# Optimization experiments

Hardware: AMD Instinct MI355X
Metric: run time of the kernel (lower is better)

## Reference

```python
import jax, jax.numpy as jnp
import numpy as np

NUM_NODES = 1024; NGRAPH = 16; N = NUM_NODES * NGRAPH
DEG = 16; E_RAND = N * DEG
F_IN = 16; EMB = 64; H = 4; C = 64; DM = H * C  # 256
NHEAD = 2; DH = DM // NHEAD; FF = 1024; OUT = 1024; NEXTRA = 3


def _p(key, shape, scale=0.05):
    return scale * jax.random.normal(key, shape, jnp.float32)


def setup_inputs() -> dict:
    key = jax.random.key(0)
    ks = iter(jax.random.split(key, 64))
    x = jax.random.normal(next(ks), (N, F_IN), jnp.float32)
    src = jax.random.randint(next(ks), (E_RAND,), 0, N, jnp.int32)
    dst = jax.random.randint(next(ks), (E_RAND,), 0, N, jnp.int32)
    loop = jnp.arange(N, dtype=jnp.int32)  # PyG GATConv add_self_loops=True
    d = {
        'x': x,
        'edge_src': jnp.concatenate([src, loop]),
        'edge_dst': jnp.concatenate([dst, loop]),
        'batch': (jnp.arange(N) // NUM_NODES).astype(jnp.int32),
        'fc1_W': _p(next(ks), (F_IN, EMB)), 'fc1_b': jnp.zeros((EMB,), jnp.float32),
        'g0_W': _p(next(ks), (EMB, DM)), 'g0_as': _p(next(ks), (H, C)),
        'g0_ad': _p(next(ks), (H, C)), 'g0_b': jnp.zeros((DM,), jnp.float32),
        'gW': _p(next(ks), (NEXTRA, DM, DM)), 'gas': _p(next(ks), (NEXTRA, H, C)),
        'gad': _p(next(ks), (NEXTRA, H, C)), 'gb': jnp.zeros((NEXTRA, DM), jnp.float32),
        'sa_Wq': _p(next(ks), (DM, DM)), 'sa_bq': jnp.zeros((DM,), jnp.float32),
        'sa_Wk': _p(next(ks), (DM, DM)), 'sa_bk': jnp.zeros((DM,), jnp.float32),
        'sa_Wv': _p(next(ks), (DM, DM)), 'sa_bv': jnp.zeros((DM,), jnp.float32),
        'sa_Wo': _p(next(ks), (DM, DM)), 'sa_bo': jnp.zeros((DM,), jnp.float32),
        'ca_Wq': _p(next(ks), (DM, DM)), 'ca_bq': jnp.zeros((DM,), jnp.float32),
        'ca_Wk': _p(next(ks), (DM, DM)), 'ca_bk': jnp.zeros((DM,), jnp.float32),
        'ca_Wv': _p(next(ks), (DM, DM)), 'ca_bv': jnp.zeros((DM,), jnp.float32),
        'ca_Wo': _p(next(ks), (DM, DM)), 'ca_bo': jnp.zeros((DM,), jnp.float32),
        'ln1_g': jnp.ones((DM,), jnp.float32), 'ln1_b': jnp.zeros((DM,), jnp.float32),
        'ln2_g': jnp.ones((DM,), jnp.float32), 'ln2_b': jnp.zeros((DM,), jnp.float32),
        'ln3_g': jnp.ones((DM,), jnp.float32), 'ln3_b': jnp.zeros((DM,), jnp.float32),
        'ff1_W': _p(next(ks), (DM, FF)), 'ff1_b': jnp.zeros((FF,), jnp.float32),
        'ff2_W': _p(next(ks), (FF, DM)), 'ff2_b': jnp.zeros((DM,), jnp.float32),
        'fc_W': _p(next(ks), (DM, OUT)), 'fc_b': jnp.zeros((OUT,), jnp.float32),
    }
    return d


def reference(x, edge_src, edge_dst, batch, fc1_W, fc1_b, g0_W, g0_as, g0_ad, g0_b,
              gW, gas, gad, gb,
              sa_Wq, sa_bq, sa_Wk, sa_bk, sa_Wv, sa_bv, sa_Wo, sa_bo,
              ca_Wq, ca_bq, ca_Wk, ca_bk, ca_Wv, ca_bv, ca_Wo, ca_bo,
              ln1_g, ln1_b, ln2_g, ln2_b, ln3_g, ln3_b,
              ff1_W, ff1_b, ff2_W, ff2_b, fc_W, fc_b):
    n = x.shape[0]

    def gat(h_in, W, a_s, a_d, b):
        h = (h_in @ W).reshape(n, H, C)                                  # [N,H,C]
        e = jax.nn.leaky_relu((h * a_s).sum(-1)[edge_src]
                              + (h * a_d).sum(-1)[edge_dst], 0.2)        # [E,H]
        m = jax.ops.segment_max(e, edge_dst, num_segments=n)
        p = jnp.exp(e - m[edge_dst])
        denom = jax.ops.segment_sum(p, edge_dst, num_segments=n)
        alpha = p / (denom[edge_dst] + 1e-16)
        out = jax.ops.segment_sum(alpha[:, :, None] * h[edge_src], edge_dst,
                                  num_segments=n)                        # [N,H,C]
        return out.reshape(n, DM) + b

    def ln(v, g, b):
        mu = v.mean(-1, keepdims=True)
        var = v.var(-1, keepdims=True)
        return (v - mu) / jnp.sqrt(var + 1e-5) * g + b

    def mha(q_in, kv_in, Wq, bq, Wk, bk, Wv, bv, Wo, bo):
        Bq, S, _ = q_in.shape
        q = (q_in @ Wq + bq).reshape(Bq, S, NHEAD, DH)
        k = (kv_in @ Wk + bk).reshape(Bq, -1, NHEAD, DH)
        v = (kv_in @ Wv + bv).reshape(Bq, -1, NHEAD, DH)
        att = jax.nn.softmax(jnp.einsum('bqhd,bkhd->bhqk', q, k) / np.float32(np.sqrt(DH)), axis=-1)
        o = jnp.einsum('bhqk,bkhd->bqhd', att, v).reshape(Bq, S, DM)
        return o @ Wo + bo

    h = x @ fc1_W + fc1_b
    h = jax.nn.leaky_relu(gat(h, g0_W, g0_as, g0_ad, g0_b), 0.01)
    for i in range(NEXTRA):
        h = jax.nn.leaky_relu(gat(h, gW[i], gas[i], gad[i], gb[i]), 0.01)

    t = h.reshape(NGRAPH, NUM_NODES, DM)
    mem = t
    t = ln(t + mha(t, t, sa_Wq, sa_bq, sa_Wk, sa_bk, sa_Wv, sa_bv, sa_Wo, sa_bo), ln1_g, ln1_b)
    t = ln(t + mha(t, mem, ca_Wq, ca_bq, ca_Wk, ca_bk, ca_Wv, ca_bv, ca_Wo, ca_bo), ln2_g, ln2_b)
    t = ln(t + (jax.nn.relu(t @ ff1_W + ff1_b) @ ff2_W + ff2_b), ln3_g, ln3_b)

    h = t.reshape(n, DM)
    cnt = jax.ops.segment_sum(jnp.ones((n,), h.dtype), batch, num_segments=NGRAPH)
    pooled = jax.ops.segment_sum(h, batch, num_segments=NGRAPH) / cnt[:, None]
    return pooled @ fc_W + fc_b
```

## Files before the change

### kernel.cpp

```cpp
#include <hip/hip_runtime.h>
#include <cstddef>

#define NNODES 16384
#define DMODEL 256
#define CCH 64
#define SQLEN 1024
#define NGRAPH 16
#define ADH 128

typedef __bf16 bf16;
typedef __attribute__((ext_vector_type(8))) __bf16 bf16x8;
typedef __attribute__((ext_vector_type(4))) __bf16 bf16x4;
typedef __attribute__((ext_vector_type(4))) float floatx4;

template <int BN>
__global__ __launch_bounds__(256) void mfma_gemm_t(
    const bf16* __restrict__ A, const bf16* __restrict__ Bt,
    const float* __restrict__ bias, float* __restrict__ Cf, bf16* __restrict__ Cb,
    int M, int N, int K, int act,
    const float* __restrict__ gas, const float* __restrict__ gad,
    float* __restrict__ ssrc, float* __restrict__ sdst)
{
  constexpr int BM = 128;
  constexpr int MW = (BN == 128) ? 4 : 2;
  constexpr int NW = 4;
  constexpr int ACH = BM / 8;
  constexpr int TCH = (BM + BN) / 8;
  __shared__ bf16 As[BM * 64];
  __shared__ bf16 Bs[BN * 64];
  const int tid = threadIdx.x;
  const int wave = tid >> 6, lane = tid & 63;
  const int m0 = blockIdx.y * BM, n0 = blockIdx.x * BN;
  const int lr = lane & 15, quad = lane >> 4;
  const int wm = (BN == 128) ? (wave >> 1) * 64 : wave * 32;
  const int wn = (BN == 128) ? (wave & 1) * 64 : 0;
  const int r8 = lane >> 3, cu = lane & 7;
  const int scol = (cu ^ r8) * 8;

  floatx4 acc[MW][NW];
  const floatx4 zero = {0.f, 0.f, 0.f, 0.f};
#pragma unroll
  for (int i = 0; i < MW; i++)
#pragma unroll
    for (int j = 0; j < NW; j++) acc[i][j] = zero;

  for (int k0 = 0; k0 < K; k0 += 64) {
#pragma unroll
    for (int c = wave; c < TCH; c += 4) {
      const bf16* g;
      bf16* l;
      if (c < ACH) {
        g = A + (size_t)(m0 + c * 8 + r8) * K + k0 + scol;
        l = &As[c * 512];
      } else {
        int c2 = c - ACH;
        g = Bt + (size_t)(n0 + c2 * 8 + r8) * K + k0 + scol;
        l = &Bs[c2 * 512];
      }
      __builtin_amdgcn_global_load_lds(
          (const __attribute__((address_space(1))) void*)g,
          (__attribute__((address_space(3))) void*)l, 16, 0, 0);
    }
    __syncthreads();
#pragma unroll
    for (int ks = 0; ks < 2; ks++) {
      bf16x8 af[MW], bfr[NW];
#pragma unroll
      for (int i = 0; i < MW; i++) {
        int row = wm + i * 16 + lr;
        af[i] = *(const bf16x8*)&As[(row * 8 + ((ks * 4 + quad) ^ (row & 7))) * 8];
      }
#pragma unroll
      for (int i = 0; i < NW; i++) {
        int row = wn + i * 16 + lr;
        bfr[i] = *(const bf16x8*)&Bs[(row * 8 + ((ks * 4 + quad) ^ (row & 7))) * 8];
      }
#pragma unroll
      for (int mi = 0; mi < MW; mi++)
#pragma unroll
        for (int ni = 0; ni < NW; ni++)
          acc[mi][ni] = __builtin_amdgcn_mfma_f32_16x16x32_bf16(af[mi], bfr[ni], acc[mi][ni], 0, 0, 0);
    }
    __syncthreads();
  }

  float as_v[4], ad_v[4];
  int head = 0;
  if (gas) {
    head = (n0 + wn) >> 6;
#pragma unroll
    for (int ni = 0; ni < 4; ni++) {
      as_v[ni] = gas[head * 64 + ni * 16 + lr];
      ad_v[ni] = gad[head * 64 + ni * 16 + lr];
    }
  }

#pragma unroll
  for (int mi = 0; mi < MW; mi++) {
    int rbase = m0 + wm + mi * 16 + quad * 4;
#pragma unroll
    for (int r = 0; r < 4; r++) {
      int row = rbase + r;
      float s1 = 0.f, s2 = 0.f;
#pragma unroll
      for (int ni = 0; ni < NW; ni++) {
        int col = n0 + wn + ni * 16 + lr;
        float v = acc[mi][ni][r];
        if (gas) { s1 += v * as_v[ni]; s2 += v * ad_v[ni]; }
        if (bias) v += bias[col];
        if (act == 1) v = fmaxf(v, 0.f);
        if (Cf) Cf[(size_t)row * N + col] = v;
        if (Cb) Cb[(size_t)row * N + col] = (bf16)v;
      }
      if (gas) {
        s1 += __shfl_xor(s1, 1); s1 += __shfl_xor(s1, 2);
        s1 += __shfl_xor(s1, 4); s1 += __shfl_xor(s1, 8);
        s2 += __shfl_xor(s2, 1); s2 += __shfl_xor(s2, 2);
        s2 += __shfl_xor(s2, 4); s2 += __shfl_xor(s2, 8);
        if (lr == 0) {
          ssrc[row * 4 + head] = s1;
          sdst[row * 4 + head] = s2;
        }
      }
    }
  }
}

struct PrepArgs {
  const float* sq[11]; bf16* dq[11];
  const float* g0W; bf16* g0Wt;
  const float* ff1W; bf16* ff1Wt;
  const float* ff2W; bf16* ff2Wt;
  const float* sabq; const float* sabk; const float* sabv;
  const float* cabk; const float* cabv;
  float* qkvb; float* kvb;
  int* cnt;
  const float* x; const float* fc1W; const float* fc1b; bf16* h0;
};

__global__ __launch_bounds__(256) void prep_kernel(PrepArgs a)
{
  __shared__ float t[32][33];
  int b = blockIdx.x;
  int tid = threadIdx.x;
  int tx = tid & 31, ty = tid >> 5;
  if (b < 704) {
    int w = b >> 6, tile = b & 63;
    int n0 = (tile & 7) * 32, k0 = (tile >> 3) * 32;
    const float* W = a.sq[w];
    bf16* Wt = a.dq[w];
#pragma unroll
    for (int i = 0; i < 4; i++) t[ty + 8 * i][tx] = W[(size_t)(k0 + ty + 8 * i) * 256 + n0 + tx];
    __syncthreads();
#pragma unroll
    for (int i = 0; i < 4; i++) Wt[(size_t)(n0 + ty + 8 * i) * 256 + k0 + tx] = (bf16)t[tx][ty + 8 * i];
  } else if (b < 720) {
    int tile = b - 704;
    int n0 = (tile & 7) * 32, k0 = (tile >> 3) * 32;
#pragma unroll
    for (int i = 0; i < 4; i++) t[ty + 8 * i][tx] = a.g0W[(size_t)(k0 + ty + 8 * i) * 256 + n0 + tx];
    __syncthreads();
#pragma unroll
    for (int i = 0; i < 4; i++) a.g0Wt[(size_t)(n0 + ty + 8 * i) * 64 + k0 + tx] = (bf16)t[tx][ty + 8 * i];
  } else if (b < 976) {
    int tile = b - 720;
    int n0 = (tile & 31) * 32, k0 = (tile >> 5) * 32;
#pragma unroll
    for (int i = 0; i < 4; i++) t[ty + 8 * i][tx] = a.ff1W[(size_t)(k0 + ty + 8 * i) * 1024 + n0 + tx];
    __syncthreads();
#pragma unroll
    for (int i = 0; i < 4; i++) a.ff1Wt[(size_t)(n0 + ty + 8 * i) * 256 + k0 + tx] = (bf16)t[tx][ty + 8 * i];
  } else if (b < 1232) {
    int tile = b - 976;
    int n0 = (tile & 7) * 32, k0 = (tile >> 3) * 32;
#pragma unroll
    for (int i = 0; i < 4; i++) t[ty + 8 * i][tx] = a.ff2W[(size_t)(k0 + ty + 8 * i) * 256 + n0 + tx];
    __syncthreads();
#pragma unroll
    for (int i = 0; i < 4; i++) a.ff2Wt[(size_t)(n0 + ty + 8 * i) * 1024 + k0 + tx] = (bf16)t[tx][ty + 8 * i];
  } else if (b == 1232) {
    a.qkvb[tid] = a.sabq[tid];
    a.qkvb[256 + tid] = a.sabk[tid];
    a.qkvb[512 + tid] = a.sabv[tid];
    a.kvb[tid] = a.cabk[tid];
    a.kvb[256 + tid] = a.cabv[tid];
  } else if (b < 1249) {
    int i0 = (b - 1233) * 1024 + tid;
#pragma unroll
    for (int i = 0; i < 4; i++) a.cnt[i0 + 256 * i] = 0;
  } else {
    int idx = (b - 1249) * 256 + tid;
    int n = idx >> 6, j = idx & 63;
    const float* xr = a.x + (size_t)n * 16;
    float s = a.fc1b[j];
#pragma unroll
    for (int k = 0; k < 16; k++) s += xr[k] * a.fc1W[k * 64 + j];
    a.h0[idx] = (bf16)s;
  }
}

__global__ __launch_bounds__(256) void vtrans2_kernel(const bf16* __restrict__ Vc, const bf16* __restrict__ Vs,
                                                      bf16* __restrict__ VtC, bf16* __restrict__ VtS)
{
  __shared__ bf16 t[32][34];
  int z = blockIdx.z;
  const bf16* V;
  bf16* Vt;
  int ldv, coff, b;
  if (z < NGRAPH) { V = Vc; Vt = VtC; ldv = 512; coff = 256; b = z; }
  else            { V = Vs; Vt = VtS; ldv = 768; coff = 512; b = z - NGRAPH; }
  int head = blockIdx.y >> 2, d0 = (blockIdx.y & 3) * 32;
  int k0 = blockIdx.x * 32;
  int tx = threadIdx.x & 31, ty = threadIdx.x >> 5;
#pragma unroll
  for (int i = 0; i < 4; i++)
    t[ty + 8 * i][tx] = V[((size_t)(b * SQLEN + k0 + ty + 8 * i)) * ldv + coff + head * ADH + d0 + tx];
  __syncthreads();
#pragma unroll
  for (int i = 0; i < 4; i++)
    Vt[((size_t)((b * 2 + head) * ADH) + d0 + ty + 8 * i) * SQLEN + k0 + tx] = t[tx][ty + 8 * i];
}

__global__ __launch_bounds__(256) void attn_mfma_kernel(
    const bf16* __restrict__ Q, int ldq, const bf16* __restrict__ K, int ldk,
    const bf16* __restrict__ Vt, bf16* __restrict__ O)
{
  const int qt = blockIdx.x, head = blockIdx.y, b = blockIdx.z;
  const int tid = threadIdx.x, wave = tid >> 6, lane = tid & 63;
  const int lr = lane & 15, quad = lane >> 4;

  __shared__ __align__(16) bf16 Ks[2][64 * 128];
  __shared__ __align__(16) bf16 Vts[2][128 * 64];
  __shared__ __align__(16) bf16 Ps[4][16][72];

  const int q0 = qt * 64 + wave * 16;
  const size_t qrow = ((size_t)b * SQLEN + q0 + lr) * ldq + head * ADH;
  const float scale2 = 0.08838834764831845f * 1.4426950408889634f;
  bf16x8 qf[4];
#pragma unroll
  for (int s = 0; s < 4; s++) {
    qf[s] = *(const bf16x8*)&Q[qrow + s * 32 + quad * 8];
#pragma unroll
    for (int j = 0; j < 8; j++) qf[s][j] = (bf16)((float)qf[s][j] * scale2);
  }

  floatx4 accO[8];
  const floatx4 zero = {0.f, 0.f, 0.f, 0.f};
#pragma unroll
  for (int n = 0; n < 8; n++) accO[n] = zero;
  float lsum = 0.f;

  const bf16* kbase = K + ((size_t)b * SQLEN) * ldk + head * ADH;
  const bf16* vtb = Vt + ((size_t)((b * 2 + head) * ADH)) * SQLEN;

  auto stage = [&](int buf, int k0) {
#pragma unroll
    for (int p = 0; p < 4; p++) {
      int bu = p * 256 + wave * 64;
      int u = bu + lane;
      int r = u >> 4, cq = u & 15;
      int c = cq ^ (r & 7);
      __builtin_amdgcn_global_load_lds(
          (const __attribute__((address_space(1))) void*)(kbase + (size_t)(k0 + r) * ldk + c * 8),
          (__attribute__((address_space(3))) void*)&Ks[buf][bu * 8], 16, 0, 0);
    }
#pragma unroll
    for (int p = 0; p < 4; p++) {
      int bu = p * 256 + wave * 64;
      int u = bu + lane;
      int r = u >> 3, cq = u & 7;
      int c = cq ^ (r & 7);
      __builtin_amdgcn_global_load_lds(
          (const __attribute__((address_space(1))) void*)(vtb + (size_t)r * SQLEN + k0 + c * 8),
          (__attribute__((address_space(3))) void*)&Vts[buf][bu * 8], 16, 0, 0);
    }
  };

  stage(0, 0);
  for (int it = 0; it < 16; it++) {
    __syncthreads();
    if (it < 15) stage((it + 1) & 1, (it + 1) * 64);
    const bf16* ks = Ks[it & 1];
    const bf16* vs = Vts[it & 1];

    floatx4 accS[4];
#pragma unroll
    for (int i = 0; i < 4; i++) accS[i] = zero;
#pragma unroll
    for (int i = 0; i < 4; i++) {
#pragma unroll
      for (int s = 0; s < 4; s++) {
        int r = i * 16 + lr;
        int cpr = (s * 4 + quad) ^ (r & 7);
        bf16x8 kf = *(const bf16x8*)&ks[(r * 16 + cpr) * 8];
        accS[i] = __builtin_amdgcn_mfma_f32_16x16x32_bf16(kf, qf[s], accS[i], 0, 0, 0);
      }
    }

#pragma unroll
    for (int i = 0; i < 4; i++) {
      bf16x4 pk;
#pragma unroll
      for (int r = 0; r < 4; r++) {
        float p = exp2f(accS[i][r]);
        pk[r] = (bf16)p;
        lsum += p;
      }
      *(bf16x4*)&Ps[wave][lr][i * 16 + quad * 4] = pk;
    }

    bf16x8 pf[2];
#pragma unroll
    for (int s = 0; s < 2; s++) pf[s] = *(const bf16x8*)&Ps[wave][lr][s * 32 + quad * 8];
#pragma unroll
    for (int n = 0; n < 8; n++) {
#pragma unroll
      for (int s = 0; s < 2; s++) {
        int r = n * 16 + lr;
        int cpr = (s * 4 + quad) ^ (r & 7);
        bf16x8 vf = *(const bf16x8*)&vs[(r * 8 + cpr) * 8];
        accO[n] = __builtin_amdgcn_mfma_f32_16x16x32_bf16(pf[s], vf, accO[n], 0, 0, 0);
      }
    }
  }

  lsum += __shfl_xor(lsum, 16);
  lsum += __shfl_xor(lsum, 32);
  float linv[4];
#pragma unroll
  for (int r = 0; r < 4; r++) linv[r] = 1.f / __shfl(lsum, quad * 4 + r);
  size_t obase = ((size_t)b * SQLEN + q0 + quad * 4) * DMODEL + head * ADH;
#pragma unroll
  for (int n = 0; n < 8; n++)
#pragma unroll
    for (int r = 0; r < 4; r++)
      O[obase + (size_t)r * DMODEL + n * 16 + lr] = (bf16)(accO[n][r] * linv[r]);
}

__global__ __launch_bounds__(256) void hist_kernel(const int* __restrict__ dst, int* __restrict__ cnt, int E)
{
  int e = blockIdx.x * 256 + threadIdx.x;
  if (e < E) atomicAdd(&cnt[dst[e]], 1);
}

__global__ __launch_bounds__(256) void scan_kernel(const int* __restrict__ cnt, int* __restrict__ offs,
                                                   int* __restrict__ cur, int n)
{
  __shared__ int partial[256];
  int tid = threadIdx.x;
  int chunk = n / 256;
  int base = tid * chunk;
  int s = 0;
  for (int i = 0; i < chunk; i++) s += cnt[base + i];
  partial[tid] = s;
  __syncthreads();
  for (int off = 1; off < 256; off <<= 1) {
    int v = 0;
    if (tid >= off) v = partial[tid - off];
    __syncthreads();
    partial[tid] += v;
    __syncthreads();
  }
  int run = partial[tid] - s;
  for (int i = 0; i < chunk; i++) {
    offs[base + i] = run;
    cur[base + i] = run;
    run += cnt[base + i];
  }
  if (tid == 255) offs[n] = run;
}

__global__ __launch_bounds__(256) void scatter_kernel(const int* __restrict__ src, const int* __restrict__ dst,
                                                      int* __restrict__ cur, int* __restrict__ csr, int E)
{
  int e = blockIdx.x * 256 + threadIdx.x;
  if (e < E) {
    int p = atomicAdd(&cur[dst[e]], 1);
    csr[p] = src[e];
  }
}

__global__ __launch_bounds__(256) void gat_fused_kernel(
    const bf16* __restrict__ hW, const int* __restrict__ offs, const int* __restrict__ csr,
    const float* __restrict__ ssrc, const float* __restrict__ sdst,
    const float* __restrict__ bias, float* __restrict__ out, bf16* __restrict__ outb)
{
  __shared__ float pL[4][128][4];
  int wave = threadIdx.x >> 6, lane = threadIdx.x & 63;
  int n = blockIdx.x * 4 + wave;
  int row0 = offs[n], row1 = offs[n + 1];
  int deg = row1 - row0;

  int src_reg = (lane < deg) ? csr[row0 + lane] : 0;

  int h1 = lane & 3, el = lane >> 2;
  float sd = sdst[n * 4 + h1];
  float m = -1e30f;
  for (int e = el; e < deg; e += 16) {
    int src = (e < 64) ? __shfl(src_reg, e) : csr[row0 + e];
    float sc = ssrc[src * 4 + h1] + sd;
    sc = (sc > 0.f) ? sc : 0.2f * sc;
    if (e < 128) pL[wave][e][h1] = sc;
    m = fmaxf(m, sc);
  }
  m = fmaxf(m, __shfl_xor(m, 4));
  m = fmaxf(m, __shfl_xor(m, 8));
  m = fmaxf(m, __shfl_xor(m, 16));
  m = fmaxf(m, __shfl_xor(m, 32));
  float den = 0.f;
  for (int e = el; e < deg; e += 16) {
    float sc;
    if (e < 128) sc = pL[wave][e][h1];
    else {
      int src = csr[row0 + e];
      sc = ssrc[src * 4 + h1] + sd;
      sc = (sc > 0.f) ? sc : 0.2f * sc;
    }
    float p = __expf(sc - m);
    if (e < 128) pL[wave][e][h1] = p;
    den += p;
  }
  den += __shfl_xor(den, 4);
  den += __shfl_xor(den, 8);
  den += __shfl_xor(den, 16);
  den += __shfl_xor(den, 32);
  float rd1 = 1.f / (den + 1e-16f);

  int h2 = lane >> 4;
  float rd = __shfl(rd1, h2);
  float m2 = __shfl(m, h2);
  float sd2 = __shfl(sd, h2);
  float4 acc = {0.f, 0.f, 0.f, 0.f};
  for (int i = 0; i < deg; i++) {
    int src = (i < 64) ? __shfl(src_reg, i) : csr[row0 + i];
    float p;
    if (i < 128) p = pL[wave][i][h2];
    else {
      float sc = ssrc[src * 4 + h2] + sd2;
      sc = (sc > 0.f) ? sc : 0.2f * sc;
      p = __expf(sc - m2);
    }
    bf16x4 hv = *(const bf16x4*)&hW[(size_t)src * DMODEL + lane * 4];
    acc.x += p * (float)hv.x; acc.y += p * (float)hv.y;
    acc.z += p * (float)hv.z; acc.w += p * (float)hv.w;
  }

  const float4 bv = *(const float4*)&bias[lane * 4];
  float v0 = acc.x * rd + bv.x, v1 = acc.y * rd + bv.y;
  float v2 = acc.z * rd + bv.z, v3 = acc.w * rd + bv.w;
  v0 = (v0 > 0.f) ? v0 : 0.01f * v0;
  v1 = (v1 > 0.f) ? v1 : 0.01f * v1;
  v2 = (v2 > 0.f) ? v2 : 0.01f * v2;
  v3 = (v3 > 0.f) ? v3 : 0.01f * v3;
  if (out) {
    float4 vout = {v0, v1, v2, v3};
    *(float4*)&out[(size_t)n * DMODEL + lane * 4] = vout;
  }
  bf16 b4[4] = {(bf16)v0, (bf16)v1, (bf16)v2, (bf16)v3};
  *(ulong1*)&outb[(size_t)n * DMODEL + lane * 4] = *(ulong1*)b4;
}

__global__ __launch_bounds__(256) void ln_kernel(
    const float* __restrict__ a, const float* __restrict__ b,
    const float* __restrict__ g, const float* __restrict__ beta,
    float* __restrict__ out, bf16* __restrict__ outb, float* __restrict__ pz)
{
  if (pz && blockIdx.x < 16) pz[blockIdx.x * 256 + threadIdx.x] = 0.f;
  int wave = threadIdx.x >> 6, lane = threadIdx.x & 63;
  int row = blockIdx.x * 4 + wave;
  const float* pa = a + (size_t)row * DMODEL;
  const float* pb = b + (size_t)row * DMODEL;
  float v[4];
  float s = 0.f;
#pragma unroll
  for (int i = 0; i < 4; i++) {
    v[i] = pa[lane + 64 * i] + pb[lane + 64 * i];
    s += v[i];
  }
#pragma unroll
  for (int o = 32; o; o >>= 1) s += __shfl_xor(s, o);
  float mu = s * (1.f / DMODEL);
  float s2 = 0.f;
#pragma unroll
  for (int i = 0; i < 4; i++) {
    float d = v[i] - mu;
    s2 += d * d;
  }
#pragma unroll
  for (int o = 32; o; o >>= 1) s2 += __shfl_xor(s2, o);
  float rstd = rsqrtf(s2 * (1.f / DMODEL) + 1e-5f);
  float* po = out + (size_t)row * DMODEL;
  bf16* pob = outb ? outb + (size_t)row * DMODEL : nullptr;
#pragma unroll
  for (int i = 0; i < 4; i++) {
    int c = lane + 64 * i;
    float ov = (v[i] - mu) * rstd * g[c] + beta[c];
    po[c] = ov;
    if (pob) pob[c] = (bf16)ov;
  }
}

__global__ __launch_bounds__(256) void pool_kernel(const float* __restrict__ t, float* __restrict__ pooled)
{
  int g = blockIdx.x, part = blockIdx.y, ch = threadIdx.x;
  int r0 = part * 128;
  float s = 0.f;
  for (int i = 0; i < 128; i++) s += t[((size_t)g * SQLEN + r0 + i) * DMODEL + ch];
  atomicAdd(&pooled[g * DMODEL + ch], s * (1.0f / 1024.0f));
}

__global__ __launch_bounds__(256) void final_fc_kernel(
    const float* __restrict__ pooled, const float* __restrict__ W,
    const float* __restrict__ b, float* __restrict__ out)
{
  int g = blockIdx.y;
  int o = blockIdx.x * 256 + threadIdx.x;
  __shared__ float p[DMODEL];
  p[threadIdx.x] = pooled[g * DMODEL + threadIdx.x];
  __syncthreads();
  float s = b[o];
#pragma unroll 8
  for (int k = 0; k < DMODEL; k++) s += p[k] * W[(size_t)k * 1024 + o];
  out[(size_t)g * 1024 + o] = s;
}

static inline void gemm(const bf16* A, const bf16* Bt, const float* bias, float* Cf, bf16* Cb,
                        int M, int N, int K, int act, hipStream_t stream,
                        const float* gas = nullptr, const float* gad = nullptr,
                        float* ssrc = nullptr, float* sdst = nullptr)
{
  if (N == 256)
    mfma_gemm_t<64><<<dim3(N / 64, M / 128), 256, 0, stream>>>(A, Bt, bias, Cf, Cb, M, N, K, act,
                                                               gas, gad, ssrc, sdst);
  else
    mfma_gemm_t<128><<<dim3(N / 128, M / 128), 256, 0, stream>>>(A, Bt, bias, Cf, Cb, M, N, K, act,
                                                                 gas, gad, ssrc, sdst);
}

extern "C" void kernel_launch(void* const* d_in, const int* in_sizes, int n_in,
                              void* d_out, int out_size, void* d_ws, size_t ws_size,
                              hipStream_t stream)
{
  const int N = NNODES;
  const float* x    = (const float*)d_in[0];
  const int* esrc   = (const int*)d_in[1];
  const int* edst   = (const int*)d_in[2];
  const int E = in_sizes[1];
  const float* fc1W = (const float*)d_in[4];
  const float* fc1b = (const float*)d_in[5];
  const float* g0W  = (const float*)d_in[6];
  const float* g0as = (const float*)d_in[7];
  const float* g0ad = (const float*)d_in[8];
  const float* g0b  = (const float*)d_in[9];
  const float* gW   = (const float*)d_in[10];
  const float* gas  = (const float*)d_in[11];
  const float* gad  = (const float*)d_in[12];
  const float* gb   = (const float*)d_in[13];
  const float* saWq = (const float*)d_in[14]; const float* sabq = (const float*)d_in[15];
  const float* saWk = (const float*)d_in[16]; const float* sabk = (const float*)d_in[17];
  const float* saWv = (const float*)d_in[18]; const float* sabv = (const float*)d_in[19];
  const float* saWo = (const float*)d_in[20]; const float* sabo = (const float*)d_in[21];
  const float* caWq = (const float*)d_in[22]; const float* cabq = (const float*)d_in[23];
  const float* caWk = (const float*)d_in[24]; const float* cabk = (const float*)d_in[25];
  const float* caWv = (const float*)d_in[26]; const float* cabv = (const float*)d_in[27];
  const float* caWo = (const float*)d_in[28]; const float* cabo = (const float*)d_in[29];
  const float* ln1g = (const float*)d_in[30]; const float* ln1b = (const float*)d_in[31];
  const float* ln2g = (const float*)d_in[32]; const float* ln2b = (const float*)d_in[33];
  const float* ln3g = (const float*)d_in[34]; const float* ln3b = (const float*)d_in[35];
  const float* ff1W = (const float*)d_in[36]; const float* ff1b = (const float*)d_in[37];
  const float* ff2W = (const float*)d_in[38]; const float* ff2b = (const float*)d_in[39];
  const float* fcW  = (const float*)d_in[40]; const float* fcb  = (const float*)d_in[41];

  float* ws = (float*)d_ws;
  const size_t NF = (size_t)N * DMODEL;
  float* A  = ws;
  float* Bb = A + NF;
  float* Kb = Bb + NF;
  bf16* P0   = (bf16*)(Kb + NF);
  bf16* P1   = P0 + NF;
  bf16* hWb  = P1 + NF;
  bf16* Bqkv = hWb + NF;
  bf16* Bkv  = Bqkv + 3 * NF;
  bf16* VtS  = Bkv + 2 * NF;
  bf16* VtC  = VtS + NF;
  bf16* Batt = VtC + NF;
  bf16* Bq   = hWb;
  bf16* FFIb = Bqkv;
  bf16* h0bf = Batt + NF;
  bf16* g0Wt = h0bf + (size_t)N * 64;
  bf16* gWt  = g0Wt + 256 * 64;
  bf16* saWqT = gWt + 3 * 65536;
  bf16* saWkT = saWqT + 65536;
  bf16* saWvT = saWkT + 65536;
  bf16* saWoT = saWvT + 65536;
  bf16* caWqT = saWoT + 65536;
  bf16* caWkT = caWqT + 65536;
  bf16* caWvT = caWkT + 65536;
  bf16* caWoT = caWvT + 65536;
  bf16* ff1Wt = caWoT + 65536;
  bf16* ff2Wt = ff1Wt + 262144;
  float* ssrc = (float*)(ff2Wt + 262144);
  float* sdst = ssrc + (size_t)N * 4;
  float* qkvb = sdst + (size_t)N * 4;
  float* kvb  = qkvb + 768;
  float* pooled = kvb + 512;
  int* cnt  = (int*)(pooled + NGRAPH * DMODEL);
  int* offs = cnt + N;
  int* cur  = offs + N + 1;
  int* csr  = cur + N;

  PrepArgs pa;
  const float* srcs[11] = {gW, gW + 65536, gW + 2 * 65536, saWq, saWk, saWv, saWo, caWq, caWk, caWv, caWo};
  bf16* dsts[11] = {gWt, gWt + 65536, gWt + 2 * 65536, saWqT, saWkT, saWvT, saWoT, caWqT, caWkT, caWvT, caWoT};
  for (int i = 0; i < 11; i++) { pa.sq[i] = srcs[i]; pa.dq[i] = dsts[i]; }
  pa.g0W = g0W; pa.g0Wt = g0Wt;
  pa.ff1W = ff1W; pa.ff1Wt = ff1Wt;
  pa.ff2W = ff2W; pa.ff2Wt = ff2Wt;
  pa.sabq = sabq; pa.sabk = sabk; pa.sabv = sabv;
  pa.cabk = cabk; pa.cabv = cabv;
  pa.qkvb = qkvb; pa.kvb = kvb;
  pa.cnt = cnt;
  pa.x = x; pa.fc1W = fc1W; pa.fc1b = fc1b; pa.h0 = h0bf;
  prep_kernel<<<1249 + (N * 64) / 256, 256, 0, stream>>>(pa);

  hist_kernel<<<(E + 255) / 256, 256, 0, stream>>>(edst, cnt, E);
  scan_kernel<<<1, 256, 0, stream>>>(cnt, offs, cur, N);
  scatter_kernel<<<(E + 255) / 256, 256, 0, stream>>>(esrc, edst, cur, csr, E);

  gemm(h0bf, g0Wt, nullptr, nullptr, hWb, N, DMODEL, 64, 0, stream, g0as, g0ad, ssrc, sdst);
  gat_fused_kernel<<<N / 4, 256, 0, stream>>>(hWb, offs, csr, ssrc, sdst, g0b, nullptr, P0);

  bf16* pin = P0; bf16* pout = P1;
  for (int i = 0; i < 3; i++) {
    gemm(pin, gWt + (size_t)i * 65536, nullptr, nullptr, hWb, N, DMODEL, DMODEL, 0, stream,
         gas + i * 256, gad + i * 256, ssrc, sdst);
    gat_fused_kernel<<<N / 4, 256, 0, stream>>>(hWb, offs, csr, ssrc, sdst, gb + i * DMODEL,
                                                (i == 2) ? A : nullptr, pout);
    bf16* tmp = pin; pin = pout; pout = tmp;
  }
  bf16* tbf = pin;

  gemm(tbf, caWkT, kvb, nullptr, Bkv, N, 512, DMODEL, 0, stream);
  gemm(tbf, saWqT, qkvb, nullptr, Bqkv, N, 768, DMODEL, 0, stream);
  vtrans2_kernel<<<dim3(32, 8, 2 * NGRAPH), 256, 0, stream>>>(Bkv, Bqkv, VtC, VtS);

  attn_mfma_kernel<<<dim3(SQLEN / 64, 2, NGRAPH), 256, 0, stream>>>(
      Bqkv, 768, Bqkv + 256, 768, VtS, Batt);
  gemm(Batt, saWoT, sabo, Bb, nullptr, N, DMODEL, DMODEL, 0, stream);
  ln_kernel<<<N / 4, 256, 0, stream>>>(A, Bb, ln1g, ln1b, Kb, P0, nullptr);

  gemm(P0, caWqT, cabq, nullptr, Bq, N, DMODEL, DMODEL, 0, stream);
  attn_mfma_kernel<<<dim3(SQLEN / 64, 2, NGRAPH), 256, 0, stream>>>(
      Bq, 256, Bkv, 512, VtC, Batt);
  gemm(Batt, caWoT, cabo, Bb, nullptr, N, DMODEL, DMODEL, 0, stream);
  ln_kernel<<<N / 4, 256, 0, stream>>>(Kb, Bb, ln2g, ln2b, A, P0, nullptr);

  gemm(P0, ff1Wt, ff1b, nullptr, FFIb, N, 1024, DMODEL, 1, stream);
  gemm(FFIb, ff2Wt, ff2b, Bb, nullptr, N, DMODEL, 1024, 0, stream);
  ln_kernel<<<N / 4, 256, 0, stream>>>(A, Bb, ln3g, ln3b, A, nullptr, pooled);

  pool_kernel<<<dim3(NGRAPH, 8), 256, 0, stream>>>(A, pooled);
  final_fc_kernel<<<dim3(4, NGRAPH), 256, 0, stream>>>(pooled, fcW, fcb, (float*)d_out);
}
```

Measured before the change: 653.2 us.

## Merge QKV and cross KV projections into one GEMM; 2-wave attention blocks

The self-attention QKV and cross-attention KV weight transposes are laid out contiguously so a single N=1280 GEMM produces all five projections into one buffer. This replaces two GEMM launches and reads the input activations once instead of twice. The attention kernel now runs 2 waves of 128 threads per block, each wave handling 32 query rows, so every K/V fragment read from LDS feeds two MFMAs. The double-buffered K/V staging is dropped in favour of a single buffer with two barriers per iteration, which trades load/compute overlap for more reuse per load and fewer threads per tile.

```diff
diff --git a/kernel.cpp b/kernel.cpp
--- a/kernel.cpp
+++ b/kernel.cpp
@@ -133,7 +133,7 @@
   const float* ff2W; bf16* ff2Wt;
   const float* sabq; const float* sabk; const float* sabv;
   const float* cabk; const float* cabv;
-  float* qkvb; float* kvb;
+  float* qkvb;
   int* cnt;
   const float* x; const float* fc1W; const float* fc1b; bf16* h0;
 };
@@ -182,8 +182,8 @@
     a.qkvb[tid] = a.sabq[tid];
     a.qkvb[256 + tid] = a.sabk[tid];
     a.qkvb[512 + tid] = a.sabv[tid];
-    a.kvb[tid] = a.cabk[tid];
-    a.kvb[256 + tid] = a.cabv[tid];
+    a.qkvb[768 + tid] = a.cabk[tid];
+    a.qkvb[1024 + tid] = a.cabv[tid];
   } else if (b < 1249) {
     int i0 = (b - 1233) * 1024 + tid;
 #pragma unroll
@@ -199,29 +199,28 @@
   }
 }
 
-__global__ __launch_bounds__(256) void vtrans2_kernel(const bf16* __restrict__ Vc, const bf16* __restrict__ Vs,
+__global__ __launch_bounds__(256) void vtrans2_kernel(const bf16* __restrict__ Bp,
                                                       bf16* __restrict__ VtC, bf16* __restrict__ VtS)
 {
   __shared__ bf16 t[32][34];
   int z = blockIdx.z;
-  const bf16* V;
   bf16* Vt;
-  int ldv, coff, b;
-  if (z < NGRAPH) { V = Vc; Vt = VtC; ldv = 512; coff = 256; b = z; }
-  else            { V = Vs; Vt = VtS; ldv = 768; coff = 512; b = z - NGRAPH; }
+  int coff, b;
+  if (z < NGRAPH) { Vt = VtC; coff = 1024; b = z; }
+  else            { Vt = VtS; coff = 512; b = z - NGRAPH; }
   int head = blockIdx.y >> 2, d0 = (blockIdx.y & 3) * 32;
   int k0 = blockIdx.x * 32;
   int tx = threadIdx.x & 31, ty = threadIdx.x >> 5;
 #pragma unroll
   for (int i = 0; i < 4; i++)
-    t[ty + 8 * i][tx] = V[((size_t)(b * SQLEN + k0 + ty + 8 * i)) * ldv + coff + head * ADH + d0 + tx];
+    t[ty + 8 * i][tx] = Bp[((size_t)(b * SQLEN + k0 + ty + 8 * i)) * 1280 + coff + head * ADH + d0 + tx];
   __syncthreads();
 #pragma unroll
   for (int i = 0; i < 4; i++)
     Vt[((size_t)((b * 2 + head) * ADH) + d0 + ty + 8 * i) * SQLEN + k0 + tx] = t[tx][ty + 8 * i];
 }
 
-__global__ __launch_bounds__(256) void attn_mfma_kernel(
+__global__ __launch_bounds__(128) void attn_mfma_kernel(
     const bf16* __restrict__ Q, int ldq, const bf16* __restrict__ K, int ldk,
     const bf16* __restrict__ Vt, bf16* __restrict__ O)
 {
@@ -229,112 +228,123 @@
   const int tid = threadIdx.x, wave = tid >> 6, lane = tid & 63;
   const int lr = lane & 15, quad = lane >> 4;
 
-  __shared__ __align__(16) bf16 Ks[2][64 * 128];
-  __shared__ __align__(16) bf16 Vts[2][128 * 64];
-  __shared__ __align__(16) bf16 Ps[4][16][72];
-
-  const int q0 = qt * 64 + wave * 16;
-  const size_t qrow = ((size_t)b * SQLEN + q0 + lr) * ldq + head * ADH;
+  __shared__ __align__(16) bf16 Ks[64 * 128];
+  __shared__ __align__(16) bf16 Vts[128 * 64];
+  __shared__ __align__(16) bf16 Ps[2][2][16][72];
+
+  const int q0 = qt * 64 + wave * 32;
   const float scale2 = 0.08838834764831845f * 1.4426950408889634f;
-  bf16x8 qf[4];
-#pragma unroll
-  for (int s = 0; s < 4; s++) {
-    qf[s] = *(const bf16x8*)&Q[qrow + s * 32 + quad * 8];
-#pragma unroll
-    for (int j = 0; j < 8; j++) qf[s][j] = (bf16)((float)qf[s][j] * scale2);
-  }
-
-  floatx4 accO[8];
+  bf16x8 qf[2][4];
+#pragma unroll
+  for (int m = 0; m < 2; m++) {
+    size_t qrow = ((size_t)b * SQLEN + q0 + m * 16 + lr) * ldq + head * ADH;
+#pragma unroll
+    for (int s = 0; s < 4; s++) {
+      qf[m][s] = *(const bf16x8*)&Q[qrow + s * 32 + quad * 8];
+#pragma unroll
+      for (int j = 0; j < 8; j++) qf[m][s][j] = (bf16)((float)qf[m][s][j] * scale2);
+    }
+  }
+
+  floatx4 accO[2][8];
   const floatx4 zero = {0.f, 0.f, 0.f, 0.f};
 #pragma unroll
-  for (int n = 0; n < 8; n++) accO[n] = zero;
-  float lsum = 0.f;
+  for (int m = 0; m < 2; m++)
+#pragma unroll
+    for (int n = 0; n < 8; n++) accO[m][n] = zero;
+  float lsum[2] = {0.f, 0.f};
 
   const bf16* kbase = K + ((size_t)b * SQLEN) * ldk + head * ADH;
   const bf16* vtb = Vt + ((size_t)((b * 2 + head) * ADH)) * SQLEN;
 
-  auto stage = [&](int buf, int k0) {
-#pragma unroll
-    for (int p = 0; p < 4; p++) {
-      int bu = p * 256 + wave * 64;
-      int u = bu + lane;
+  for (int it = 0; it < 16; it++) {
+    int k0 = it * 64;
+#pragma unroll
+    for (int p = 0; p < 8; p++) {
+      int u = p * 128 + tid;
       int r = u >> 4, cq = u & 15;
       int c = cq ^ (r & 7);
       __builtin_amdgcn_global_load_lds(
           (const __attribute__((address_space(1))) void*)(kbase + (size_t)(k0 + r) * ldk + c * 8),
-          (__attribute__((address_space(3))) void*)&Ks[buf][bu * 8], 16, 0, 0);
-    }
-#pragma unroll
-    for (int p = 0; p < 4; p++) {
-      int bu = p * 256 + wave * 64;
-      int u = bu + lane;
+          (__attribute__((address_space(3))) void*)&Ks[u * 8], 16, 0, 0);
+    }
+#pragma unroll
+    for (int p = 0; p < 8; p++) {
+      int u = p * 128 + tid;
       int r = u >> 3, cq = u & 7;
       int c = cq ^ (r & 7);
       __builtin_amdgcn_global_load_lds(
           (const __attribute__((address_space(1))) void*)(vtb + (size_t)r * SQLEN + k0 + c * 8),
-          (__attribute__((address_space(3))) void*)&Vts[buf][bu * 8], 16, 0, 0);
-    }
-  };
-
-  stage(0, 0);
-  for (int it = 0; it < 16; it++) {
-    __syncthreads();
-    if (it < 15) stage((it + 1) & 1, (it + 1) * 64);
-    const bf16* ks = Ks[it & 1];
-    const bf16* vs = Vts[it & 1];
-
-    floatx4 accS[4];
-#pragma unroll
-    for (int i = 0; i < 4; i++) accS[i] = zero;
+          (__attribute__((address_space(3))) void*)&Vts[u * 8], 16, 0, 0);
+    }
+    __syncthreads();
+
+    floatx4 accS[2][4];
+#pragma unroll
+    for (int m = 0; m < 2; m++)
+#pragma unroll
+      for (int i = 0; i < 4; i++) accS[m][i] = zero;
 #pragma unroll
     for (int i = 0; i < 4; i++) {
 #pragma unroll
       for (int s = 0; s < 4; s++) {
         int r = i * 16 + lr;
         int cpr = (s * 4 + quad) ^ (r & 7);
-        bf16x8 kf = *(const bf16x8*)&ks[(r * 16 + cpr) * 8];
-        accS[i] = __builtin_amdgcn_mfma_f32_16x16x32_bf16(kf, qf[s], accS[i], 0, 0, 0);
-      }
-    }
-
-#pragma unroll
-    for (int i = 0; i < 4; i++) {
-      bf16x4 pk;
-#pragma unroll
-      for (int r = 0; r < 4; r++) {
-        float p = exp2f(accS[i][r]);
-        pk[r] = (bf16)p;
-        lsum += p;
-      }
-      *(bf16x4*)&Ps[wave][lr][i * 16 + quad * 4] = pk;
-    }
-
-    bf16x8 pf[2];
-#pragma unroll
-    for (int s = 0; s < 2; s++) pf[s] = *(const bf16x8*)&Ps[wave][lr][s * 32 + quad * 8];
+        bf16x8 kf = *(const bf16x8*)&Ks[(r * 16 + cpr) * 8];
+        accS[0][i] = __builtin_amdgcn_mfma_f32_16x16x32_bf16(kf, qf[0][s], accS[0][i], 0, 0, 0);
+        accS[1][i] = __builtin_amdgcn_mfma_f32_16x16x32_bf16(kf, qf[1][s], accS[1][i], 0, 0, 0);
+      }
+    }
+
+#pragma unroll
+    for (int m = 0; m < 2; m++) {
+#pragma unroll
+      for (int i = 0; i < 4; i++) {
+        bf16x4 pk;
+#pragma unroll
+        for (int r = 0; r < 4; r++) {
+          float p = exp2f(accS[m][i][r]);
+          pk[r] = (bf16)p;
+          lsum[m] += p;
+        }
+        *(bf16x4*)&Ps[wave][m][lr][i * 16 + quad * 4] = pk;
+      }
+    }
+
+    bf16x8 pf[2][2];
+#pragma unroll
+    for (int m = 0; m < 2; m++)
+#pragma unroll
+      for (int s = 0; s < 2; s++) pf[m][s] = *(const bf16x8*)&Ps[wave][m][lr][s * 32 + quad * 8];
 #pragma unroll
     for (int n = 0; n < 8; n++) {
 #pragma unroll
       for (int s = 0; s < 2; s++) {
         int r = n * 16 + lr;
         int cpr = (s * 4 + quad) ^ (r & 7);
-        bf16x8 vf = *(const bf16x8*)&vs[(r * 8 + cpr) * 8];
-        accO[n] = __builtin_amdgcn_mfma_f32_16x16x32_bf16(pf[s], vf, accO[n], 0, 0, 0);
-      }
-    }
-  }
-
-  lsum += __shfl_xor(lsum, 16);
-  lsum += __shfl_xor(lsum, 32);
-  float linv[4];
-#pragma unroll
-  for (int r = 0; r < 4; r++) linv[r] = 1.f / __shfl(lsum, quad * 4 + r);
-  size_t obase = ((size_t)b * SQLEN + q0 + quad * 4) * DMODEL + head * ADH;
-#pragma unroll
-  for (int n = 0; n < 8; n++)
-#pragma unroll
-    for (int r = 0; r < 4; r++)
-      O[obase + (size_t)r * DMODEL + n * 16 + lr] = (bf16)(accO[n][r] * linv[r]);
+        bf16x8 vf = *(const bf16x8*)&Vts[(r * 8 + cpr) * 8];
+        accO[0][n] = __builtin_amdgcn_mfma_f32_16x16x32_bf16(pf[0][s], vf, accO[0][n], 0, 0, 0);
+        accO[1][n] = __builtin_amdgcn_mfma_f32_16x16x32_bf16(pf[1][s], vf, accO[1][n], 0, 0, 0);
+      }
+    }
+    __syncthreads();
+  }
+
+#pragma unroll
+  for (int m = 0; m < 2; m++) {
+    float l = lsum[m];
+    l += __shfl_xor(l, 16);
+    l += __shfl_xor(l, 32);
+    float linv[4];
+#pragma unroll
+    for (int r = 0; r < 4; r++) linv[r] = 1.f / __shfl(l, quad * 4 + r);
+    size_t obase = ((size_t)b * SQLEN + q0 + m * 16 + quad * 4) * DMODEL + head * ADH;
+#pragma unroll
+    for (int n = 0; n < 8; n++)
+#pragma unroll
+      for (int r = 0; r < 4; r++)
+        O[obase + (size_t)r * DMODEL + n * 16 + lr] = (bf16)(accO[m][n][r] * linv[r]);
+  }
 }
 
 __global__ __launch_bounds__(256) void hist_kernel(const int* __restrict__ dst, int* __restrict__ cnt, int E)
@@ -579,31 +589,25 @@
   bf16* P0   = (bf16*)(Kb + NF);
   bf16* P1   = P0 + NF;
   bf16* hWb  = P1 + NF;
-  bf16* Bqkv = hWb + NF;
-  bf16* Bkv  = Bqkv + 3 * NF;
-  bf16* VtS  = Bkv + 2 * NF;
+  bf16* Bp   = hWb + NF;
+  bf16* VtS  = Bp + 5 * NF;
   bf16* VtC  = VtS + NF;
   bf16* Batt = VtC + NF;
   bf16* Bq   = hWb;
-  bf16* FFIb = Bqkv;
+  bf16* FFIb = Bp;
   bf16* h0bf = Batt + NF;
   bf16* g0Wt = h0bf + (size_t)N * 64;
   bf16* gWt  = g0Wt + 256 * 64;
-  bf16* saWqT = gWt + 3 * 65536;
-  bf16* saWkT = saWqT + 65536;
-  bf16* saWvT = saWkT + 65536;
-  bf16* saWoT = saWvT + 65536;
+  bf16* pjWt = gWt + 3 * 65536;
+  bf16* saWoT = pjWt + 5 * 65536;
   bf16* caWqT = saWoT + 65536;
-  bf16* caWkT = caWqT + 65536;
-  bf16* caWvT = caWkT + 65536;
-  bf16* caWoT = caWvT + 65536;
+  bf16* caWoT = caWqT + 65536;
   bf16* ff1Wt = caWoT + 65536;
   bf16* ff2Wt = ff1Wt + 262144;
   float* ssrc = (float*)(ff2Wt + 262144);
   float* sdst = ssrc + (size_t)N * 4;
   float* qkvb = sdst + (size_t)N * 4;
-  float* kvb  = qkvb + 768;
-  float* pooled = kvb + 512;
+  float* pooled = qkvb + 1280;
   int* cnt  = (int*)(pooled + NGRAPH * DMODEL);
   int* offs = cnt + N;
   int* cur  = offs + N + 1;
@@ -611,14 +615,18 @@
 
   PrepArgs pa;
   const float* srcs[11] = {gW, gW + 65536, gW + 2 * 65536, saWq, saWk, saWv, saWo, caWq, caWk, caWv, caWo};
-  bf16* dsts[11] = {gWt, gWt + 65536, gWt + 2 * 65536, saWqT, saWkT, saWvT, saWoT, caWqT, caWkT, caWvT, caWoT};
+  bf16* dsts[11] = {gWt, gWt + 65536, gWt + 2 * 65536,
+                    pjWt, pjWt + 65536, pjWt + 2 * 65536,
+                    saWoT, caWqT,
+                    pjWt + 3 * 65536, pjWt + 4 * 65536,
+                    caWoT};
   for (int i = 0; i < 11; i++) { pa.sq[i] = srcs[i]; pa.dq[i] = dsts[i]; }
   pa.g0W = g0W; pa.g0Wt = g0Wt;
   pa.ff1W = ff1W; pa.ff1Wt = ff1Wt;
   pa.ff2W = ff2W; pa.ff2Wt = ff2Wt;
   pa.sabq = sabq; pa.sabk = sabk; pa.sabv = sabv;
   pa.cabk = cabk; pa.cabv = cabv;
-  pa.qkvb = qkvb; pa.kvb = kvb;
+  pa.qkvb = qkvb;
   pa.cnt = cnt;
   pa.x = x; pa.fc1W = fc1W; pa.fc1b = fc1b; pa.h0 = h0bf;
   prep_kernel<<<1249 + (N * 64) / 256, 256, 0, stream>>>(pa);
@@ -640,18 +648,17 @@
   }
   bf16* tbf = pin;
 
-  gemm(tbf, caWkT, kvb, nullptr, Bkv, N, 512, DMODEL, 0, stream);
-  gemm(tbf, saWqT, qkvb, nullptr, Bqkv, N, 768, DMODEL, 0, stream);
-  vtrans2_kernel<<<dim3(32, 8, 2 * NGRAPH), 256, 0, stream>>>(Bkv, Bqkv, VtC, VtS);
-
-  attn_mfma_kernel<<<dim3(SQLEN / 64, 2, NGRAPH), 256, 0, stream>>>(
-      Bqkv, 768, Bqkv + 256, 768, VtS, Batt);
+  gemm(tbf, pjWt, qkvb, nullptr, Bp, N, 1280, DMODEL, 0, stream);
+  vtrans2_kernel<<<dim3(32, 8, 2 * NGRAPH), 256, 0, stream>>>(Bp, VtC, VtS);
+
+  attn_mfma_kernel<<<dim3(SQLEN / 64, 2, NGRAPH), 128, 0, stream>>>(
+      Bp, 1280, Bp + 256, 1280, VtS, Batt);
   gemm(Batt, saWoT, sabo, Bb, nullptr, N, DMODEL, DMODEL, 0, stream);
   ln_kernel<<<N / 4, 256, 0, stream>>>(A, Bb, ln1g, ln1b, Kb, P0, nullptr);
 
   gemm(P0, caWqT, cabq, nullptr, Bq, N, DMODEL, DMODEL, 0, stream);
-  attn_mfma_kernel<<<dim3(SQLEN / 64, 2, NGRAPH), 256, 0, stream>>>(
-      Bq, 256, Bkv, 512, VtC, Batt);
+  attn_mfma_kernel<<<dim3(SQLEN / 64, 2, NGRAPH), 128, 0, stream>>>(
+      Bq, 256, Bp + 768, 1280, VtC, Batt);
   gemm(Batt, caWoT, cabo, Bb, nullptr, N, DMODEL, DMODEL, 0, stream);
   ln_kernel<<<N / 4, 256, 0, stream>>>(Kb, Bb, ln2g, ln2b, A, P0, nullptr);
 
```

Result: slower. 672.0 us (+2.9%).
